# Kernel tuning notes

Measured on AMD Instinct MI355X. Metric: run time of the kernel, lower is better.

Reference implementation:

```python
import jax, jax.numpy as jnp
import numpy as np
from jax import lax


def setup_inputs() -> dict:
    key = jax.random.key(0)
    ks = jax.random.split(key, 12)
    B, L, C = 256, 1024, 16
    F = C * ((L + 10 * L) // 2)  # 90112
    inp = {
        "x": jax.random.normal(ks[0], (B, L), jnp.float32),
        "leaf_w": jax.random.normal(ks[1], (L, C), jnp.float32) * 0.05,
        "leaf_b": jax.random.normal(ks[2], (L, C), jnp.float32) * 0.05,
        "conv_w": jax.random.normal(ks[3], (C, C, 3), jnp.float32) * 0.05,
        "conv_b": jax.random.normal(ks[4], (C,), jnp.float32) * 0.05,
        "bn_gamma": jnp.ones((C,), jnp.float32),
        "bn_beta": jnp.zeros((C,), jnp.float32),
        "node_weights": jax.random.uniform(ks[5], (2 * L - 1,), jnp.float32),
        "fc1_w": jax.random.normal(ks[6], (128, F), jnp.float32) * 0.01,
        "fc1_b": jax.random.normal(ks[7], (128,), jnp.float32) * 0.01,
        "fc2_w": jax.random.normal(ks[8], (64, 128), jnp.float32) * 0.05,
        "fc2_b": jax.random.normal(ks[9], (64,), jnp.float32) * 0.05,
        "fc3_w": jax.random.normal(ks[10], (1, 64), jnp.float32) * 0.05,
        "fc3_b": jax.random.normal(ks[11], (1,), jnp.float32) * 0.05,
    }
    return inp


def reference(x, leaf_w, leaf_b, conv_w, conv_b, bn_gamma, bn_beta,
              node_weights, fc1_w, fc1_b, fc2_w, fc2_b, fc3_w, fc3_b):
    B, L = x.shape
    C = leaf_w.shape[1]
    D = int(np.log2(L))  # perfect binary tree depth
    EPS = 1e-5

    # per-leaf 1x1 conv (distinct weights per leaf) + per-leaf node weight
    leaf = x[:, :, None] * leaf_w[None] + leaf_b[None]           # [B,L,C]
    leaf = leaf * node_weights[:L][None, :, None]
    all_feats = [jnp.transpose(leaf, (0, 2, 1))]                  # [B,C,L] (leaf length 1 each)

    bn_scale = bn_gamma / jnp.sqrt(1.0 + EPS)                     # eval-mode BN (mean=0, var=1)

    X = leaf[:, :, :, None]                                       # [B,N,C,len]
    offset = L
    for _ in range(D):
        Bn, N, Cc, Lk = X.shape
        N2 = N // 2
        # concat sibling pairs along length
        Y = X.reshape(Bn, N2, 2, Cc, Lk).transpose(0, 1, 3, 2, 4).reshape(Bn, N2, Cc, 2 * Lk)
        Z = Y.reshape(Bn * N2, Cc, 2 * Lk)
        Z = lax.conv_general_dilated(Z, conv_w, window_strides=(1,), padding="SAME",
                                     dimension_numbers=("NCH", "OIH", "NCH"))
        Z = Z + conv_b[None, :, None]
        Z = Z * bn_scale[None, :, None] + bn_beta[None, :, None]
        Z = jax.nn.relu(Z)
        Z = Z.reshape(Bn, N2, Cc, 2 * Lk)
        Z = Z * node_weights[offset:offset + N2][None, :, None, None]
        offset += N2
        all_feats.append(Z.transpose(0, 2, 1, 3).reshape(Bn, Cc, N2 * 2 * Lk))
        X = Z

    comb = jnp.concatenate(all_feats, axis=2)                     # [B,C,T]
    T = comb.shape[2]
    pooled = comb[:, :, : (T // 2) * 2].reshape(B, C, T // 2, 2).max(-1)  # MaxPool1d(2)
    flat = pooled.reshape(B, -1)
    h = jax.nn.relu(flat @ fc1_w.T + fc1_b)
    h = jax.nn.relu(h @ fc2_w.T + fc2_b)
    return h @ fc3_w.T + fc3_b
```

## Files before the change

### kernel.cpp

```cpp
#include <hip/hip_runtime.h>
#include <hip/hip_bf16.h>

#define BATCH 256
#define L 1024
#define C 16
#define POOL 512
#define PCOLS 5632
#define FDIM 90112
#define H1 128
#define H2 64

#define KS 256
#define KCHUNK (FDIM / KS)

#define SROW 24
#define SBUF (1025 * SROW)
#define TREE_LDS_BYTES (2 * SBUF * 2 + 2047 * 4)

typedef float f32x4 __attribute__((ext_vector_type(4)));
typedef short bf16x8 __attribute__((ext_vector_type(8)));
typedef unsigned long long u64;

__device__ __forceinline__ unsigned short f2b(float f) {
    union { __hip_bfloat16 h; unsigned short u; } cv;
    cv.h = __float2bfloat16(f);
    return cv.u;
}
__device__ __forceinline__ unsigned int pk(float lo, float hi) {
    return (unsigned int)f2b(lo) | ((unsigned int)f2b(hi) << 16);
}

__launch_bounds__(1024, 4)
__global__ void tree_kernel(const float* __restrict__ x,
                            const float* __restrict__ leaf_w,
                            const float* __restrict__ leaf_b,
                            const float* __restrict__ conv_w,
                            const float* __restrict__ conv_b,
                            const float* __restrict__ bn_gamma,
                            const float* __restrict__ bn_beta,
                            const float* __restrict__ node_w,
                            unsigned short* __restrict__ pooledb,
                            const float* __restrict__ w1,
                            unsigned short* __restrict__ w1p) {
    extern __shared__ short smem[];
    short* buf0 = smem;
    short* buf1 = smem + SBUF;
    float* nwl  = (float*)(smem + 2 * SBUF);

    const int b   = blockIdx.x;
    const int tid = threadIdx.x;
    const int lane = tid & 63;
    const int wv   = tid >> 6;
    const int n    = lane & 15;
    const int g    = lane >> 4;

    if (tid < SROW) {
        buf0[1024 * SROW + tid] = 0;
        buf1[1024 * SROW + tid] = 0;
    }
    for (int i = tid; i < 2047; i += 1024) nwl[i] = node_w[i];

    bf16x8 A1, A2;
#pragma unroll
    for (int j = 0; j < 8; ++j) {
        const int ci = (g & 1) * 8 + j;
        A1[j] = (short)f2b(conv_w[(n * C + ci) * 3 + (g >> 1)]);
        A2[j] = (g < 2) ? (short)f2b(conv_w[(n * C + ci) * 3 + 2]) : (short)0;
    }
    const float scn = bn_gamma[n] / sqrtf(1.0f + 1e-5f);
    const float btn = conv_b[n] * scn + bn_beta[n];

    const int gbase = b * 11264 + tid;

    {
        const float xv = x[b * L + tid];
        const float nw = node_w[tid];
        const float4* lwa = (const float4*)(leaf_w + 16 * tid);
        const float4* lba = (const float4*)(leaf_b + 16 * tid);
        short* row = buf0 + tid * SROW;
#pragma unroll 1
        for (int q = 0; q < 4; ++q) {
            float4 wq = lwa[q], bq = lba[q];
            float v0 = (xv * wq.x + bq.x) * nw;
            float v1 = (xv * wq.y + bq.y) * nw;
            float v2 = (xv * wq.z + bq.z) * nw;
            float v3 = (xv * wq.w + bq.w) * nw;
            *(u64*)(row + 4 * q) =
                (u64)pk(v0, v1) | ((u64)pk(v2, v3) << 32);
            float p0 = fmaxf(v0, __shfl_xor(v0, 1));
            float p1 = fmaxf(v1, __shfl_xor(v1, 1));
            float p2 = fmaxf(v2, __shfl_xor(v2, 1));
            float p3 = fmaxf(v3, __shfl_xor(v3, 1));
            if (!(tid & 1)) {
                *(u64*)(pooledb + (long)b * FDIM + (tid >> 1) * 16 + 4 * q) =
                    (u64)pk(p0, p1) | ((u64)pk(p2, p3) << 32);
            }
        }
        __syncthreads();
    }

    short* bin  = buf0;
    short* bout = buf1;
    int noff = L;
    for (int d = 0; d < 10; ++d) {
        const int sh = d + 1;
        const int mask = (1 << sh) - 1;

        {
            const int gidx = gbase + d * 1024;
            const int pos2 = gidx & 511;
            const int c4   = (gidx >> 9) & 3;
            const int un   = gidx >> 11;
            const int lev  = un >> 7;
            const int nr   = un & 127;
            const float* src = w1 + (long)nr * FDIM + lev * POOL + pos2;
            float f0 = src[(c4 * 4 + 0) * PCOLS];
            float f1 = src[(c4 * 4 + 1) * PCOLS];
            float f2 = src[(c4 * 4 + 2) * PCOLS];
            float f3 = src[(c4 * 4 + 3) * PCOLS];
            *(u64*)(w1p + (long)nr * FDIM + lev * 8192 + pos2 * 16 + c4 * 4) =
                (u64)pk(f0, f1) | ((u64)pk(f2, f3) << 32);
        }

        bf16x8 B1s[4], B2s[4];
#pragma unroll
        for (int ti = 0; ti < 4; ++ti) {
            const int pos = (wv * 4 + ti) * 16 + n;
            const bool ok1 = (g >= 2) || ((pos & mask) != 0);
            const int r1 = ok1 ? (pos + (g >> 1) - 1) : 1024;
            B1s[ti] = *(const bf16x8*)(bin + r1 * SROW + (g & 1) * 8);
            const bool ok2 = ((pos & mask) != mask);
            const int r2 = ok2 ? (pos + 1) : 1024;
            B2s[ti] = *(const bf16x8*)(bin + r2 * SROW + (g & 1) * 8);
        }

#pragma unroll
        for (int ti = 0; ti < 4; ++ti) {
            const int base = (wv * 4 + ti) * 16 + 4 * g;

            f32x4 acc = {0.f, 0.f, 0.f, 0.f};
            acc = __builtin_amdgcn_mfma_f32_16x16x32_bf16(B1s[ti], A1, acc, 0, 0, 0);
            acc = __builtin_amdgcn_mfma_f32_16x16x32_bf16(B2s[ti], A2, acc, 0, 0, 0);

            float z[4];
#pragma unroll
            for (int r = 0; r < 4; ++r) {
                const float nwv = nwl[noff + ((base + r) >> sh)];
                z[r] = fmaxf(fmaf(scn, acc[r], btn), 0.f) * nwv;
            }

            if (d < 9) {
#pragma unroll
                for (int r = 0; r < 4; ++r)
                    bout[(base + r) * SROW + n] = (short)f2b(z[r]);
            }

            const int pos2 = base >> 1;
            unsigned short* pp = pooledb + (long)b * FDIM + sh * 8192 + pos2 * 16 + n;
            pp[0]  = f2b(fmaxf(z[0], z[1]));
            pp[16] = f2b(fmaxf(z[2], z[3]));
        }

        if (d >= 5 && d < 9) {
            __syncthreads();
        } else {
            asm volatile("s_waitcnt lgkmcnt(0)" ::: "memory");
        }

        short* t = bin; bin = bout; bout = t;
        noff += (512 >> d);
    }

    {
        const int gidx = gbase + 10 * 1024;
        const int pos2 = gidx & 511;
        const int c4   = (gidx >> 9) & 3;
        const int un   = gidx >> 11;
        const int lev  = un >> 7;
        const int nr   = un & 127;
        const float* src = w1 + (long)nr * FDIM + lev * POOL + pos2;
        float f0 = src[(c4 * 4 + 0) * PCOLS];
        float f1 = src[(c4 * 4 + 1) * PCOLS];
        float f2 = src[(c4 * 4 + 2) * PCOLS];
        float f3 = src[(c4 * 4 + 3) * PCOLS];
        *(u64*)(w1p + (long)nr * FDIM + lev * 8192 + pos2 * 16 + c4 * 4) =
            (u64)pk(f0, f1) | ((u64)pk(f2, f3) << 32);
    }
}

__launch_bounds__(512, 2)
__global__ void fc1_mfma(const unsigned short* __restrict__ pooledb,
                         const unsigned short* __restrict__ w1b,
                         unsigned int* __restrict__ p32) {
    const int ks  = blockIdx.x;

    const int tid  = threadIdx.x;
    const int wv   = tid >> 6;
    const int lane = tid & 63;
    const int lrow = lane & 15;
    const int lk   = (lane >> 4) * 8;

    const int m0 = wv * 32;
    const int kb = ks * KCHUNK;

    const unsigned short* ap0 = pooledb + (long)(m0 + lrow) * FDIM + kb + lk;
    const unsigned short* ap1 = ap0 + (long)16 * FDIM;
    const unsigned short* bp  = w1b + (long)lrow * FDIM + kb + lk;

    f32x4 acc[2][8];
#pragma unroll
    for (int i = 0; i < 2; ++i)
#pragma unroll
        for (int ct = 0; ct < 8; ++ct) acc[i][ct] = (f32x4){0.f, 0.f, 0.f, 0.f};

#pragma unroll 1
    for (int kk = 0; kk < KCHUNK; kk += 32) {
        bf16x8 a0 = *(const bf16x8*)(ap0 + kk);
        bf16x8 a1 = *(const bf16x8*)(ap1 + kk);
#pragma unroll
        for (int ct = 0; ct < 8; ++ct) {
            bf16x8 bv = *(const bf16x8*)(bp + (long)(ct * 16) * FDIM + kk);
            acc[0][ct] = __builtin_amdgcn_mfma_f32_16x16x32_bf16(a0, bv, acc[0][ct], 0, 0, 0);
            acc[1][ct] = __builtin_amdgcn_mfma_f32_16x16x32_bf16(a1, bv, acc[1][ct], 0, 0, 0);
        }
    }

    const int rbase = (lane >> 4) * 4;
    const int half  = lane & 1;
    const int cpair = (lane & 15) >> 1;
#pragma unroll
    for (int r = 0; r < 4; ++r) {
        const int row = m0 + (half << 4) + rbase + r;
        unsigned int* p = p32 + (long)row * (KS * 64) + ks * 64 + cpair;
#pragma unroll
        for (int ct = 0; ct < 8; ++ct) {
            float x0 = acc[0][ct][r], x1 = acc[1][ct][r];
            float y0 = __shfl_xor(x0, 1), y1 = __shfl_xor(x1, 1);
            float lo = half ? y1 : x0;
            float hi = half ? x1 : y0;
            p[ct * 8] = pk(lo, hi);
        }
    }
}

__launch_bounds__(1024)
__global__ void fc_tail(const unsigned int* __restrict__ p32,
                        const float* __restrict__ fc1_b,
                        const float* __restrict__ w2,
                        const float* __restrict__ b2,
                        const float* __restrict__ w3,
                        const float* __restrict__ b3,
                        float* __restrict__ out) {
    __shared__ float red[16][H1];
    __shared__ float h1_s[H1];
    __shared__ float w2_s[H2 * 129];

    const int b = blockIdx.x;
    const int tid = threadIdx.x;
    const int t2 = tid & 63;
    const int q  = tid >> 6;

    float s0 = 0.f, s1 = 0.f;
    const unsigned int* pb = p32 + (long)b * (KS * 64) + (q * 16) * 64 + t2;
#pragma unroll
    for (int kt = 0; kt < 16; ++kt) {
        unsigned int v = pb[kt * 64];
        union { unsigned int u; float f; } lo, hi;
        lo.u = v << 16;
        hi.u = v & 0xffff0000u;
        s0 += lo.f;
        s1 += hi.f;
    }
    red[q][2 * t2]     = s0;
    red[q][2 * t2 + 1] = s1;

    for (int i = tid; i < H2 * H1; i += 1024) {
        int j = i >> 7, k = i & 127;
        w2_s[j * 129 + k] = w2[i];
    }
    __syncthreads();

    if (tid < 128) {
        float ss = 0.f;
#pragma unroll
        for (int qq = 0; qq < 16; ++qq) ss += red[qq][tid];
        h1_s[tid] = fmaxf(ss + fc1_b[tid], 0.f);
    }
    __syncthreads();

    if (tid < 64) {
        float a2 = 0.f;
#pragma unroll 8
        for (int k = 0; k < H1; ++k) a2 = fmaf(h1_s[k], w2_s[tid * 129 + k], a2);
        float h2 = fmaxf(a2 + b2[tid], 0.f);
        float r = h2 * w3[tid];
#pragma unroll
        for (int off = 32; off > 0; off >>= 1) r += __shfl_down(r, off);
        if (tid == 0) out[b] = r + b3[0];
    }
}

extern "C" void kernel_launch(void* const* d_in, const int* in_sizes, int n_in,
                              void* d_out, int out_size, void* d_ws, size_t ws_size,
                              hipStream_t stream) {
    const float* x        = (const float*)d_in[0];
    const float* leaf_w   = (const float*)d_in[1];
    const float* leaf_b   = (const float*)d_in[2];
    const float* conv_w   = (const float*)d_in[3];
    const float* conv_b   = (const float*)d_in[4];
    const float* bn_gamma = (const float*)d_in[5];
    const float* bn_beta  = (const float*)d_in[6];
    const float* node_w   = (const float*)d_in[7];
    const float* fc1_w    = (const float*)d_in[8];
    const float* fc1_b    = (const float*)d_in[9];
    const float* fc2_w    = (const float*)d_in[10];
    const float* fc2_b    = (const float*)d_in[11];
    const float* fc3_w    = (const float*)d_in[12];
    const float* fc3_b    = (const float*)d_in[13];

    unsigned short* pooledb = (unsigned short*)d_ws;
    unsigned short* w1p     = pooledb + (long)BATCH * FDIM;
    unsigned int*   p32     = (unsigned int*)(w1p + (long)H1 * FDIM);

    (void)hipFuncSetAttribute((const void*)tree_kernel,
                        hipFuncAttributeMaxDynamicSharedMemorySize, TREE_LDS_BYTES);

    tree_kernel<<<BATCH, 1024, TREE_LDS_BYTES, stream>>>(
        x, leaf_w, leaf_b, conv_w, conv_b, bn_gamma, bn_beta, node_w, pooledb,
        fc1_w, w1p);

    fc1_mfma<<<KS, 512, 0, stream>>>(pooledb, w1p, p32);

    fc_tail<<<BATCH, 1024, 0, stream>>>(p32, fc1_b, fc2_w, fc2_b, fc3_w, fc3_b,
                                        (float*)d_out);
}
```

Baseline: 74.93 us.

## Split tree kernel into half-row blocks plus separate final-level kernel

Each batch row's tree is split across two 512-thread blocks that handle levels 0-8 on independent halves, since those levels never cross the midpoint. The final level, which spans the whole row, moves to a new kernel that reads level-8 outputs from a global scratch buffer. The aim is more blocks and half the LDS per block for better occupancy and more parallelism, at the cost of an extra launch and a global round trip for level 8.

Result: slower. 85.15 us (+13.6%).

```diff
diff --git a/kernel.cpp b/kernel.cpp
--- a/kernel.cpp
+++ b/kernel.cpp
@@ -14,8 +14,9 @@
 #define KCHUNK (FDIM / KS)
 
 #define SROW 24
-#define SBUF (1025 * SROW)
-#define TREE_LDS_BYTES (2 * SBUF * 2 + 2047 * 4)
+#define HROWS 513
+#define HBUFS (HROWS * SROW)
+#define T8_LDS_BYTES (2 * HBUFS * 2 + 2047 * 4)
 
 typedef float f32x4 __attribute__((ext_vector_type(4)));
 typedef short bf16x8 __attribute__((ext_vector_type(8)));
@@ -30,35 +31,38 @@
     return (unsigned int)f2b(lo) | ((unsigned int)f2b(hi) << 16);
 }
 
-__launch_bounds__(1024, 4)
-__global__ void tree_kernel(const float* __restrict__ x,
-                            const float* __restrict__ leaf_w,
-                            const float* __restrict__ leaf_b,
-                            const float* __restrict__ conv_w,
-                            const float* __restrict__ conv_b,
-                            const float* __restrict__ bn_gamma,
-                            const float* __restrict__ bn_beta,
-                            const float* __restrict__ node_w,
-                            unsigned short* __restrict__ pooledb,
-                            const float* __restrict__ w1,
-                            unsigned short* __restrict__ w1p) {
+__launch_bounds__(512, 4)
+__global__ void tree08(const float* __restrict__ x,
+                       const float* __restrict__ leaf_w,
+                       const float* __restrict__ leaf_b,
+                       const float* __restrict__ conv_w,
+                       const float* __restrict__ conv_b,
+                       const float* __restrict__ bn_gamma,
+                       const float* __restrict__ bn_beta,
+                       const float* __restrict__ node_w,
+                       unsigned short* __restrict__ pooledb,
+                       const float* __restrict__ w1,
+                       unsigned short* __restrict__ w1p,
+                       unsigned short* __restrict__ glvl8) {
     extern __shared__ short smem[];
     short* buf0 = smem;
-    short* buf1 = smem + SBUF;
-    float* nwl  = (float*)(smem + 2 * SBUF);
-
-    const int b   = blockIdx.x;
+    short* buf1 = smem + HBUFS;
+    float* nwl  = (float*)(smem + 2 * HBUFS);
+
+    const int bid = blockIdx.x;
+    const int b   = bid >> 1;
+    const int h   = bid & 1;
     const int tid = threadIdx.x;
     const int lane = tid & 63;
-    const int wv   = tid >> 6;
+    const int wvv  = tid >> 6;
     const int n    = lane & 15;
     const int g    = lane >> 4;
 
     if (tid < SROW) {
-        buf0[1024 * SROW + tid] = 0;
-        buf1[1024 * SROW + tid] = 0;
-    }
-    for (int i = tid; i < 2047; i += 1024) nwl[i] = node_w[i];
+        buf0[512 * SROW + tid] = 0;
+        buf1[512 * SROW + tid] = 0;
+    }
+    for (int i = tid; i < 2047; i += 512) nwl[i] = node_w[i];
 
     bf16x8 A1, A2;
 #pragma unroll
@@ -70,13 +74,12 @@
     const float scn = bn_gamma[n] / sqrtf(1.0f + 1e-5f);
     const float btn = conv_b[n] * scn + bn_beta[n];
 
-    const int gbase = b * 11264 + tid;
-
     {
-        const float xv = x[b * L + tid];
-        const float nw = node_w[tid];
-        const float4* lwa = (const float4*)(leaf_w + 16 * tid);
-        const float4* lba = (const float4*)(leaf_b + 16 * tid);
+        const int gp = h * 512 + tid;
+        const float xv = x[b * L + gp];
+        const float nw = node_w[gp];
+        const float4* lwa = (const float4*)(leaf_w + 16 * gp);
+        const float4* lba = (const float4*)(leaf_b + 16 * gp);
         short* row = buf0 + tid * SROW;
 #pragma unroll 1
         for (int q = 0; q < 4; ++q) {
@@ -92,7 +95,7 @@
             float p2 = fmaxf(v2, __shfl_xor(v2, 1));
             float p3 = fmaxf(v3, __shfl_xor(v3, 1));
             if (!(tid & 1)) {
-                *(u64*)(pooledb + (long)b * FDIM + (tid >> 1) * 16 + 4 * q) =
+                *(u64*)(pooledb + (long)b * FDIM + (gp >> 1) * 16 + 4 * q) =
                     (u64)pk(p0, p1) | ((u64)pk(p2, p3) << 32);
             }
         }
@@ -102,12 +105,12 @@
     short* bin  = buf0;
     short* bout = buf1;
     int noff = L;
-    for (int d = 0; d < 10; ++d) {
+    for (int d = 0; d < 9; ++d) {
         const int sh = d + 1;
         const int mask = (1 << sh) - 1;
 
         {
-            const int gidx = gbase + d * 1024;
+            const int gidx = (bid * 11 + d) * 512 + tid;
             const int pos2 = gidx & 511;
             const int c4   = (gidx >> 9) & 3;
             const int un   = gidx >> 11;
@@ -125,18 +128,19 @@
         bf16x8 B1s[4], B2s[4];
 #pragma unroll
         for (int ti = 0; ti < 4; ++ti) {
-            const int pos = (wv * 4 + ti) * 16 + n;
-            const bool ok1 = (g >= 2) || ((pos & mask) != 0);
-            const int r1 = ok1 ? (pos + (g >> 1) - 1) : 1024;
+            const int lp = (wvv * 4 + ti) * 16 + n;
+            const bool ok1 = (g >= 2) || ((lp & mask) != 0);
+            const int r1 = ok1 ? (lp + (g >> 1) - 1) : 512;
             B1s[ti] = *(const bf16x8*)(bin + r1 * SROW + (g & 1) * 8);
-            const bool ok2 = ((pos & mask) != mask);
-            const int r2 = ok2 ? (pos + 1) : 1024;
+            const bool ok2 = ((lp & mask) != mask);
+            const int r2 = ok2 ? (lp + 1) : 512;
             B2s[ti] = *(const bf16x8*)(bin + r2 * SROW + (g & 1) * 8);
         }
 
 #pragma unroll
         for (int ti = 0; ti < 4; ++ti) {
-            const int base = (wv * 4 + ti) * 16 + 4 * g;
+            const int base = (wvv * 4 + ti) * 16 + 4 * g;
+            const int gb   = h * 512 + base;
 
             f32x4 acc = {0.f, 0.f, 0.f, 0.f};
             acc = __builtin_amdgcn_mfma_f32_16x16x32_bf16(B1s[ti], A1, acc, 0, 0, 0);
@@ -145,25 +149,30 @@
             float z[4];
 #pragma unroll
             for (int r = 0; r < 4; ++r) {
-                const float nwv = nwl[noff + ((base + r) >> sh)];
+                const float nwv = nwl[noff + ((gb + r) >> sh)];
                 z[r] = fmaxf(fmaf(scn, acc[r], btn), 0.f) * nwv;
             }
 
-            if (d < 9) {
+            if (d < 8) {
 #pragma unroll
                 for (int r = 0; r < 4; ++r)
                     bout[(base + r) * SROW + n] = (short)f2b(z[r]);
+            } else {
+                unsigned short* gp8 = glvl8 + ((long)b * L + gb) * 16 + n;
+#pragma unroll
+                for (int r = 0; r < 4; ++r)
+                    gp8[r * 16] = f2b(z[r]);
             }
 
-            const int pos2 = base >> 1;
+            const int pos2 = gb >> 1;
             unsigned short* pp = pooledb + (long)b * FDIM + sh * 8192 + pos2 * 16 + n;
             pp[0]  = f2b(fmaxf(z[0], z[1]));
             pp[16] = f2b(fmaxf(z[2], z[3]));
         }
 
-        if (d >= 5 && d < 9) {
+        if (d >= 5 && d < 8) {
             __syncthreads();
-        } else {
+        } else if (d < 8) {
             asm volatile("s_waitcnt lgkmcnt(0)" ::: "memory");
         }
 
@@ -171,8 +180,9 @@
         noff += (512 >> d);
     }
 
-    {
-        const int gidx = gbase + 10 * 1024;
+#pragma unroll
+    for (int j = 9; j < 11; ++j) {
+        const int gidx = (bid * 11 + j) * 512 + tid;
         const int pos2 = gidx & 511;
         const int c4   = (gidx >> 9) & 3;
         const int un   = gidx >> 11;
@@ -185,6 +195,61 @@
         float f3 = src[(c4 * 4 + 3) * PCOLS];
         *(u64*)(w1p + (long)nr * FDIM + lev * 8192 + pos2 * 16 + c4 * 4) =
             (u64)pk(f0, f1) | ((u64)pk(f2, f3) << 32);
+    }
+}
+
+__launch_bounds__(512, 4)
+__global__ void tree9(const unsigned short* __restrict__ glvl8,
+                      const float* __restrict__ conv_w,
+                      const float* __restrict__ conv_b,
+                      const float* __restrict__ bn_gamma,
+                      const float* __restrict__ bn_beta,
+                      const float* __restrict__ node_w,
+                      unsigned short* __restrict__ pooledb) {
+    const int b   = blockIdx.x;
+    const int tid = threadIdx.x;
+    const int lane = tid & 63;
+    const int wvv  = tid >> 6;
+    const int n    = lane & 15;
+    const int g    = lane >> 4;
+
+    bf16x8 A1, A2;
+#pragma unroll
+    for (int j = 0; j < 8; ++j) {
+        const int ci = (g & 1) * 8 + j;
+        A1[j] = (short)f2b(conv_w[(n * C + ci) * 3 + (g >> 1)]);
+        A2[j] = (g < 2) ? (short)f2b(conv_w[(n * C + ci) * 3 + 2]) : (short)0;
+    }
+    const float scn = bn_gamma[n] / sqrtf(1.0f + 1e-5f);
+    const float btn = conv_b[n] * scn + bn_beta[n];
+    const float nwv = node_w[2046];
+
+    const unsigned short* base8 = glvl8 + (long)b * L * 16;
+    const bf16x8 zero = {0, 0, 0, 0, 0, 0, 0, 0};
+
+#pragma unroll 1
+    for (int ti = 0; ti < 8; ++ti) {
+        const int pos = (wvv * 8 + ti) * 16 + n;
+        const bool ok1 = (g >= 2) || (pos != 0);
+        const int r1 = pos + (g >> 1) - 1;
+        bf16x8 B1 = ok1 ? *(const bf16x8*)(base8 + (long)r1 * 16 + (g & 1) * 8) : zero;
+        const bool ok2 = (pos != L - 1);
+        bf16x8 B2 = ok2 ? *(const bf16x8*)(base8 + (long)(pos + 1) * 16 + (g & 1) * 8) : zero;
+
+        f32x4 acc = {0.f, 0.f, 0.f, 0.f};
+        acc = __builtin_amdgcn_mfma_f32_16x16x32_bf16(B1, A1, acc, 0, 0, 0);
+        acc = __builtin_amdgcn_mfma_f32_16x16x32_bf16(B2, A2, acc, 0, 0, 0);
+
+        const int cb = (wvv * 8 + ti) * 16 + 4 * g;
+        float z[4];
+#pragma unroll
+        for (int r = 0; r < 4; ++r)
+            z[r] = fmaxf(fmaf(scn, acc[r], btn), 0.f) * nwv;
+
+        const int pos2 = cb >> 1;
+        unsigned short* pp = pooledb + (long)b * FDIM + 10 * 8192 + pos2 * 16 + n;
+        pp[0]  = f2b(fmaxf(z[0], z[1]));
+        pp[16] = f2b(fmaxf(z[2], z[3]));
     }
 }
 
@@ -321,13 +386,17 @@
     unsigned short* pooledb = (unsigned short*)d_ws;
     unsigned short* w1p     = pooledb + (long)BATCH * FDIM;
     unsigned int*   p32     = (unsigned int*)(w1p + (long)H1 * FDIM);
-
-    (void)hipFuncSetAttribute((const void*)tree_kernel,
-                        hipFuncAttributeMaxDynamicSharedMemorySize, TREE_LDS_BYTES);
-
-    tree_kernel<<<BATCH, 1024, TREE_LDS_BYTES, stream>>>(
+    unsigned short* glvl8   = (unsigned short*)(p32 + (long)BATCH * KS * 64);
+
+    (void)hipFuncSetAttribute((const void*)tree08,
+                        hipFuncAttributeMaxDynamicSharedMemorySize, T8_LDS_BYTES);
+
+    tree08<<<BATCH * 2, 512, T8_LDS_BYTES, stream>>>(
         x, leaf_w, leaf_b, conv_w, conv_b, bn_gamma, bn_beta, node_w, pooledb,
-        fc1_w, w1p);
+        fc1_w, w1p, glvl8);
+
+    tree9<<<BATCH, 512, 0, stream>>>(glvl8, conv_w, conv_b, bn_gamma, bn_beta,
+                                     node_w, pooledb);
 
     fc1_mfma<<<KS, 512, 0, stream>>>(pooledb, w1p, p32);
 
```
